# Performance work log

Measured on AMD Instinct MI355X. Metric: run time of the kernel, lower is better.

The kernel has to match this reference:

```python
import jax, jax.numpy as jnp
import numpy as np
import math

B, S, D = 2, 2048, 1024
H = 16
HD = D // H          # 64
ROT = HD             # rotary_pct = 1.0 -> full head dim
BASE = 10000.0


def _rotate_half(x):
    half = x.shape[-1] // 2
    return jnp.concatenate([-x[..., half:], x[..., :half]], axis=-1)


def _cos_sin(seq_len, dtype):
    inv_freq = 1.0 / (BASE ** (jnp.arange(0, ROT, 2, dtype=jnp.float32) / ROT))
    t = jnp.arange(seq_len, dtype=jnp.float32)
    freqs = jnp.einsum('i,j->ij', t, inv_freq)            # [S, ROT/2]
    emb = jnp.concatenate([freqs, freqs], axis=-1)        # [S, ROT]
    return jnp.cos(emb).astype(dtype)[None, None], jnp.sin(emb).astype(dtype)[None, None]


def setup_inputs() -> dict:
    key = jax.random.key(0)
    k1, k2, k3 = jax.random.split(key, 3)
    x = jax.random.normal(k1, (B, S, D), dtype=jnp.float32)
    attn_mask = jnp.ones((B, S), dtype=jnp.int32)
    W_qkv = jax.random.normal(k2, (3 * D, D), dtype=jnp.float32) * 0.02
    W_out = jax.random.normal(k3, (D, D), dtype=jnp.float32) * 0.02
    return {"x": x, "attn_mask": attn_mask, "W_qkv": W_qkv, "W_out": W_out}


def reference(x, attn_mask, W_qkv, W_out):
    bsz, seq_len, _ = x.shape
    dtype = x.dtype
    neg = jnp.finfo(dtype).min

    qkv = jnp.einsum('bsd,ed->bse', x, W_qkv)                     # [B,S,3D]
    qkv = qkv.reshape(bsz, seq_len, 3, H, HD).transpose(2, 0, 3, 1, 4)
    q, k, v = qkv[0], qkv[1], qkv[2]                              # [B,H,S,HD]

    cos, sin = _cos_sin(seq_len, dtype)                           # [1,1,S,ROT]
    q = q * cos + _rotate_half(q) * sin
    k = k * cos + _rotate_half(k) * sin

    scores = jnp.einsum('bhqd,bhkd->bhqk', q, k) / math.sqrt(HD)  # [B,H,S,S]
    causal = jnp.tril(jnp.ones((seq_len, seq_len), dtype=bool))
    scores = jnp.where(causal[None, None], scores, neg)
    # 2D padding mask over key positions
    scores = jnp.where((attn_mask[:, None, None, :] == 0), neg, scores)

    attn = jax.nn.softmax(scores, axis=-1)
    out = jnp.einsum('bhqk,bhkd->bhqd', attn, v)                  # [B,H,S,HD]
    out = out.transpose(0, 2, 1, 3).reshape(bsz, seq_len, D)
    return jnp.einsum('bsd,ed->bse', out, W_out)
```

## Files before the change

kernel.cpp:

```cpp
#include <hip/hip_runtime.h>
#include <hip/hip_bf16.h>
#include <math.h>
#include <stdint.h>

typedef __hip_bfloat16 bf16;
typedef __attribute__((ext_vector_type(8))) short short8;
typedef __attribute__((ext_vector_type(4))) float f32x4;
typedef __attribute__((ext_vector_type(16))) float f32x16;

#define NB 2
#define NS 2048
#define ND 1024
#define NH 16
#define NHD 64
#define N3D 3072

#define SM_SCALE 0.18033688011112042f

__device__ __forceinline__ void gload16(const bf16* g, void* l) {
  __builtin_amdgcn_global_load_lds(
      (const __attribute__((address_space(1))) uint32_t*)g,
      (__attribute__((address_space(3))) uint32_t*)l, 16, 0, 0);
}

__global__ void cast3_kernel(const float4* __restrict__ x, bf16* __restrict__ xb,
                             const float4* __restrict__ wq, bf16* __restrict__ wqb,
                             const float4* __restrict__ wo, bf16* __restrict__ wob) {
  int i = blockIdx.x * blockDim.x + threadIdx.x;
  const float4* src;
  bf16* dst;
  int off;
  if (i < 1048576) {
    src = x; dst = xb; off = i;
  } else if (i < 1835008) {
    src = wq; dst = wqb; off = i - 1048576;
  } else {
    src = wo; dst = wob; off = i - 1835008;
  }
  float4 v = src[off];
  alignas(8) bf16 r[4];
  r[0] = __float2bfloat16(v.x);
  r[1] = __float2bfloat16(v.y);
  r[2] = __float2bfloat16(v.z);
  r[3] = __float2bfloat16(v.w);
  *reinterpret_cast<uint2*>(dst + (size_t)off * 4) = *reinterpret_cast<const uint2*>(r);
}

__global__ void ropetab_kernel(float* __restrict__ cs_tab, float* __restrict__ sn_tab) {
  int idx = blockIdx.x * blockDim.x + threadIdx.x;
  int j = idx & 31;
  int s = idx >> 5;
  float inv = exp2f((float)(2 * j) * (-13.287712379549449f / 64.0f));
  float ang = (float)s * inv;
  float sn, cs;
  sincosf(ang, &sn, &cs);
  cs_tab[idx] = cs;
  sn_tab[idx] = sn;
}

#define GEMM_PIPE_BODY(...)                                                               \
  __shared__ short As[3][128 * 64];                                                       \
  __shared__ short Bs[3][128 * 64];                                                       \
  const int tid = threadIdx.x;                                                            \
  const int lane = tid & 63;                                                              \
  const int w = tid >> 6;                                                                 \
  const int wm = w >> 2, wn = w & 3;                                                      \
  const int l15 = lane & 15, l4 = lane >> 4;                                              \
  const int r0 = tid >> 3, seg = tid & 7;                                                 \
  const int sw = ((seg ^ (r0 & 7)) << 3);                                                 \
  const bf16* Ar0 = Ap + (size_t)(bm0 + r0) * 1024 + sw;                                  \
  const bf16* Ar1 = Ap + (size_t)(bm0 + r0 + 64) * 1024 + sw;                             \
  const bf16* Br0 = Bp + (size_t)(bn0 + r0) * 1024 + sw;                                  \
  const bf16* Br1 = Bp + (size_t)(bn0 + r0 + 64) * 1024 + sw;                             \
  f32x4 acc[4][2] = {};                                                                   \
  gload16(Ar0 + 0, &As[0][w * 512]);                                                      \
  gload16(Ar1 + 0, &As[0][4096 + w * 512]);                                               \
  gload16(Br0 + 0, &Bs[0][w * 512]);                                                      \
  gload16(Br1 + 0, &Bs[0][4096 + w * 512]);                                               \
  gload16(Ar0 + 64, &As[1][w * 512]);                                                     \
  gload16(Ar1 + 64, &As[1][4096 + w * 512]);                                              \
  gload16(Br0 + 64, &Bs[1][w * 512]);                                                     \
  gload16(Br1 + 64, &Bs[1][4096 + w * 512]);                                              \
  asm volatile("s_waitcnt vmcnt(4)" ::: "memory");                                        \
  __builtin_amdgcn_s_barrier();                                                           \
  for (int t = 0; t < 16; ++t) {                                                          \
    const int slot = t % 3;                                                               \
    if (t + 2 < 16) {                                                                     \
      const int ns = (t + 2) % 3;                                                         \
      const int nk = (t + 2) * 64;                                                        \
      gload16(Ar0 + nk, &As[ns][w * 512]);                                                \
      gload16(Ar1 + nk, &As[ns][4096 + w * 512]);                                         \
      gload16(Br0 + nk, &Bs[ns][w * 512]);                                                \
      gload16(Br1 + nk, &Bs[ns][4096 + w * 512]);                                         \
    }                                                                                     \
    _Pragma("unroll") for (int kk = 0; kk < 2; ++kk) {                                    \
      short8 af[4], bfr[2];                                                               \
      _Pragma("unroll") for (int mi = 0; mi < 4; ++mi) {                                  \
        int row = wm * 64 + mi * 16 + l15;                                                \
        af[mi] = *(const short8*)&As[slot][row * 64 + (((kk * 4 + l4) ^ (row & 7)) << 3)];\
      }                                                                                   \
      _Pragma("unroll") for (int ni = 0; ni < 2; ++ni) {                                  \
        int row = (wn >> 1) * 64 + (wn & 1) * 16 + ni * 32 + l15;                         \
        bfr[ni] = *(const short8*)&Bs[slot][row * 64 + (((kk * 4 + l4) ^ (row & 7)) << 3)];\
      }                                                                                   \
      __builtin_amdgcn_s_setprio(1);                                                      \
      _Pragma("unroll") for (int mi = 0; mi < 4; ++mi)                                    \
        _Pragma("unroll") for (int ni = 0; ni < 2; ++ni)                                  \
          acc[mi][ni] =                                                                   \
              __builtin_amdgcn_mfma_f32_16x16x32_bf16(af[mi], bfr[ni], acc[mi][ni], 0, 0, 0);\
      __builtin_amdgcn_s_setprio(0);                                                      \
    }                                                                                     \
    if (t + 2 < 16) {                                                                     \
      asm volatile("s_waitcnt vmcnt(4)" ::: "memory");                                    \
      __builtin_amdgcn_s_barrier();                                                       \
    } else if (t < 15) {                                                                  \
      asm volatile("s_waitcnt vmcnt(0)" ::: "memory");                                    \
      __builtin_amdgcn_s_barrier();                                                       \
    }                                                                                     \
  }                                                                                       \
  __VA_ARGS__

__global__ __launch_bounds__(512) void gemm_qkv(const bf16* __restrict__ Ap,
                                                const bf16* __restrict__ Bp,
                                                const float* __restrict__ cs_tab,
                                                const float* __restrict__ sn_tab,
                                                bf16* __restrict__ Qr, bf16* __restrict__ Kr,
                                                bf16* __restrict__ Vt) {
  const int lin = blockIdx.x;
  const int xcd = lin & 7, idx = lin >> 3;
  const int bxx = (xcd & 1) * 12 + idx % 12;
  const int byy = (xcd >> 1) * 8 + idx / 12;
  const int bn0 = bxx * 128, bm0 = byy * 128;
  GEMM_PIPE_BODY(
    const int colw = bn0 + (wn >> 1) * 64 + (wn & 1) * 16;
    if (bn0 < 2048) {
      bf16* dst = (colw >> 10) ? Kr : Qr;
      const int h = (colw & 1023) >> 6;
      const int j = (wn & 1) * 16 + l15;
      _Pragma("unroll") for (int mi = 0; mi < 4; ++mi) {
        _Pragma("unroll") for (int r = 0; r < 4; ++r) {
          int row = bm0 + wm * 64 + mi * 16 + l4 * 4 + r;
          int b = row >> 11;
          int s = row & (NS - 1);
          float cs = cs_tab[s * 32 + j];
          float sn = sn_tab[s * 32 + j];
          float v0 = acc[mi][0][r];
          float v1 = acc[mi][1][r];
          size_t base = ((size_t)(b * NH + h) * NS + s) * NHD + j;
          dst[base] = __float2bfloat16(v0 * cs - v1 * sn);
          dst[base + 32] = __float2bfloat16(v1 * cs + v0 * sn);
        }
      }
    } else {
      __syncthreads();
      bf16* vtile = reinterpret_cast<bf16*>(&As[0][0]);
      _Pragma("unroll") for (int mi = 0; mi < 4; ++mi) {
        _Pragma("unroll") for (int ni = 0; ni < 2; ++ni) {
          _Pragma("unroll") for (int r = 0; r < 4; ++r) {
            int srow = wm * 64 + mi * 16 + l4 * 4 + r;
            int c = (wn >> 1) * 64 + (wn & 1) * 16 + ni * 32 + l15;
            vtile[c * 136 + srow] = __float2bfloat16(acc[mi][ni][r]);
          }
        }
      }
      __syncthreads();
      const int b_ = bm0 >> 11;
      const int s0 = (bm0 & (NS - 1)) + (tid & 3) * 32;
      const int c = tid >> 2;
      const int head = ((bn0 - 2048) >> 6) + (c >> 6);
      bf16* dstp = Vt + (((size_t)(b_ * NH + head)) * NHD + (c & 63)) * NS + s0;
      _Pragma("unroll") for (int g = 0; g < 4; ++g)
        *reinterpret_cast<short8*>(dstp + g * 8) =
            *reinterpret_cast<const short8*>(&vtile[c * 136 + (tid & 3) * 32 + g * 8]);
    }
  )
}

__global__ __launch_bounds__(512) void gemm_bt(const bf16* __restrict__ Ap,
                                               const bf16* __restrict__ Bp,
                                               float* __restrict__ Cv) {
  const int lin = blockIdx.x;
  const int xcd = lin & 7, idx = lin >> 3;
  const int bxx = (xcd & 1) * 4 + (idx & 3);
  const int byy = (xcd >> 1) * 8 + (idx >> 2);
  const int bn0 = bxx * 128, bm0 = byy * 128;
  GEMM_PIPE_BODY(
    _Pragma("unroll") for (int mi = 0; mi < 4; ++mi) {
      _Pragma("unroll") for (int ni = 0; ni < 2; ++ni) {
        _Pragma("unroll") for (int r = 0; r < 4; ++r) {
          int row = bm0 + wm * 64 + mi * 16 + l4 * 4 + r;
          int col = bn0 + (wn >> 1) * 64 + (wn & 1) * 16 + ni * 32 + l15;
          Cv[(size_t)row * ND + col] = acc[mi][ni][r];
        }
      }
    }
  )
}

__global__ void maskbias_kernel(const int* __restrict__ amask, float* __restrict__ mb, int n) {
  int i = blockIdx.x * blockDim.x + threadIdx.x;
  if (i < n) mb[i] = amask[i] ? 0.f : -1e30f;
}

__global__ __launch_bounds__(256, 2) void attn_kernel(const bf16* __restrict__ Qr,
                                                      const bf16* __restrict__ Kr,
                                                      const bf16* __restrict__ Vt,
                                                      const float* __restrict__ mb,
                                                      bf16* __restrict__ AO) {
  __shared__ short Ks[2][64 * 64];
  __shared__ short Vs[2][64 * 64];
  __shared__ float Mb[2][64];

  const int tid = threadIdx.x;
  const int lane = tid & 63;
  const int w = tid >> 6;
  const int q = lane & 31;
  const int hi = lane >> 5;

  const int lin = blockIdx.x;
  const int xcd = lin & 7;
  const int k = lin >> 3;
  const int bh = xcd * 4 + (k & 3);
  const int kk = k >> 2;
  const int tile = (k < 32) ? (15 - kk) : (kk - 8);
  const int b = bh >> 4, h = bh & 15;
  const int qw = tile * 128 + w * 32;
  const int nc = 2 * tile + 2;

  const bf16* Qb = Qr + (size_t)bh * NS * NHD;
  const bf16* Kb = Kr + (size_t)bh * NS * NHD;
  const bf16* Vb = Vt + (size_t)bh * NHD * NS;

  const int srow = tid >> 2;
  const int sc0 = (tid & 3) * 16;
  const int swz = (srow & 7) << 3;

  short8 Qf[4];
#pragma unroll
  for (int s = 0; s < 4; ++s)
    Qf[s] = *reinterpret_cast<const short8*>(&Qb[(size_t)(qw + q) * NHD + s * 16 + hi * 8]);

  f32x16 o0 = {}, o1 = {};
  float mx = -1e30f, lsum = 0.f;

  short8 kreg[2], vreg[2];
  float4 mreg;
  auto prefetch = [&](int kv0) {
    kreg[0] = *reinterpret_cast<const short8*>(&Kb[(size_t)(kv0 + srow) * NHD + sc0]);
    kreg[1] = *reinterpret_cast<const short8*>(&Kb[(size_t)(kv0 + srow) * NHD + sc0 + 8]);
    vreg[0] = *reinterpret_cast<const short8*>(&Vb[(size_t)srow * NS + kv0 + sc0]);
    vreg[1] = *reinterpret_cast<const short8*>(&Vb[(size_t)srow * NS + kv0 + sc0 + 8]);
    if (tid < 16) mreg = *reinterpret_cast<const float4*>(&mb[b * NS + kv0 + tid * 4]);
  };
  auto stage = [&](int buf) {
    *reinterpret_cast<short8*>(&Ks[buf][srow * 64 + (sc0 ^ swz)]) = kreg[0];
    *reinterpret_cast<short8*>(&Ks[buf][srow * 64 + ((sc0 + 8) ^ swz)]) = kreg[1];
    *reinterpret_cast<short8*>(&Vs[buf][srow * 64 + (sc0 ^ swz)]) = vreg[0];
    *reinterpret_cast<short8*>(&Vs[buf][srow * 64 + ((sc0 + 8) ^ swz)]) = vreg[1];
    if (tid < 16) *reinterpret_cast<float4*>(&Mb[buf][tid * 4]) = mreg;
  };

  prefetch(0);
  stage(0);
  __syncthreads();

  const int rsw = (q & 7) << 3;

  for (int c = 0; c < nc; ++c) {
    const int cur = c & 1;
    const int kv0 = c * 64;
    if (c + 1 < nc) prefetch((c + 1) * 64);

    if (kv0 < qw + 32) {
      f32x16 a0 = {}, a1 = {};
#pragma unroll
      for (int s = 0; s < 4; ++s) {
        short8 kf0 = *reinterpret_cast<const short8*>(
            &Ks[cur][q * 64 + ((s * 16 + hi * 8) ^ rsw)]);
        short8 kf1 = *reinterpret_cast<const short8*>(
            &Ks[cur][(32 + q) * 64 + ((s * 16 + hi * 8) ^ rsw)]);
        a0 = __builtin_amdgcn_mfma_f32_32x32x16_bf16(kf0, Qf[s], a0, 0, 0, 0);
        a1 = __builtin_amdgcn_mfma_f32_32x32x16_bf16(kf1, Qf[s], a1, 0, 0, 0);
      }

      float4 bv[2][4];
#pragma unroll
      for (int t = 0; t < 2; ++t)
#pragma unroll
        for (int g = 0; g < 4; ++g)
          bv[t][g] = *reinterpret_cast<const float4*>(&Mb[cur][t * 32 + g * 8 + hi * 4]);
      const int qg = qw + q;
#pragma unroll
      for (int t = 0; t < 2; ++t) {
        f32x16& a = t ? a1 : a0;
        const bool needc = (kv0 + t * 32 + 31 > qw);
#pragma unroll
        for (int r = 0; r < 16; ++r) {
          float v = fmaf(a[r], SM_SCALE, ((const float*)&bv[t][r >> 2])[r & 3]);
          if (needc) {
            int kvg = kv0 + t * 32 + (r & 3) + 8 * (r >> 2) + 4 * hi;
            if (kvg > qg) v = -1e30f;
          }
          a[r] = v;
        }
      }

      float cm = a0[0];
#pragma unroll
      for (int r = 1; r < 16; ++r) cm = fmaxf(cm, a0[r]);
#pragma unroll
      for (int r = 0; r < 16; ++r) cm = fmaxf(cm, a1[r]);
      float pm = fmaxf(cm, __shfl_xor(cm, 32));

      if (!__all(pm <= mx + 8.f)) {
        float mn = fmaxf(mx, pm);
        float fac = __builtin_amdgcn_exp2f(mx - mn);
        mx = mn;
        lsum *= fac;
#pragma unroll
        for (int r = 0; r < 16; ++r) {
          float fq = __shfl(fac, (r & 3) + 8 * (r >> 2) + 4 * hi);
          o0[r] *= fq;
          o1[r] *= fq;
        }
      }

      float rs = 0.f;
      short8 pa[4];
#pragma unroll
      for (int t = 0; t < 2; ++t) {
        f32x16& a = t ? a1 : a0;
#pragma unroll
        for (int r = 0; r < 16; ++r) {
          float e = __builtin_amdgcn_exp2f(a[r] - mx);
          a[r] = e;
          rs += e;
        }
#pragma unroll
        for (int g = 0; g < 2; ++g) {
          union { unsigned int u; __hip_bfloat162 h2; } X, X2, Y, Y2;
          X.h2 = __float22bfloat162_rn(float2{a[g * 8 + 0], a[g * 8 + 1]});
          X2.h2 = __float22bfloat162_rn(float2{a[g * 8 + 2], a[g * 8 + 3]});
          Y.h2 = __float22bfloat162_rn(float2{a[g * 8 + 4], a[g * 8 + 5]});
          Y2.h2 = __float22bfloat162_rn(float2{a[g * 8 + 6], a[g * 8 + 7]});
          asm volatile("v_permlane32_swap_b32 %0, %1" : "+v"(X.u), "+v"(Y.u));
          asm volatile("v_permlane32_swap_b32 %0, %1" : "+v"(X2.u), "+v"(Y2.u));
          union { unsigned int u[4]; short8 s; } P;
          P.u[0] = X.u;
          P.u[1] = X2.u;
          P.u[2] = Y.u;
          P.u[3] = Y2.u;
          pa[t * 2 + g] = P.s;
        }
      }
      lsum += rs + __shfl_xor(rs, 32);

#pragma unroll
      for (int ks = 0; ks < 4; ++ks) {
        const int vcol = (ks * 16 + hi * 8) ^ rsw;
        short8 vf0 = *reinterpret_cast<const short8*>(&Vs[cur][q * 64 + vcol]);
        short8 vf1 = *reinterpret_cast<const short8*>(&Vs[cur][(32 + q) * 64 + vcol]);
        o0 = __builtin_amdgcn_mfma_f32_32x32x16_bf16(pa[ks], vf0, o0, 0, 0, 0);
        o1 = __builtin_amdgcn_mfma_f32_32x32x16_bf16(pa[ks], vf1, o1, 0, 0, 0);
      }
    }

    if (c + 1 < nc) stage(cur ^ 1);
    __syncthreads();
  }

  float inv = 1.0f / lsum;
#pragma unroll
  for (int r = 0; r < 16; ++r) {
    const int crow = (r & 3) + 8 * (r >> 2) + 4 * hi;
    float iq = __shfl(inv, crow);
    size_t base = (size_t)(b * NS + qw + crow) * ND + h * NHD;
    AO[base + q] = __float2bfloat16(o0[r] * iq);
    AO[base + 32 + q] = __float2bfloat16(o1[r] * iq);
  }
}

extern "C" void kernel_launch(void* const* d_in, const int* in_sizes, int n_in,
                              void* d_out, int out_size, void* d_ws, size_t ws_size,
                              hipStream_t stream) {
  const float* x = (const float*)d_in[0];
  const int* amask = (const int*)d_in[1];
  const float* Wqkv = (const float*)d_in[2];
  const float* Wout = (const float*)d_in[3];
  float* out = (float*)d_out;

  char* p = (char*)d_ws;
  bf16* xb = (bf16*)(p);
  bf16* wqkvb = (bf16*)(p + 8388608);
  bf16* woutb = (bf16*)(p + 14680064);
  float* cs_tab = (float*)(p + 25165824);
  float* sn_tab = (float*)(p + 25427968);
  float* mbias = (float*)(p + 25690112);
  bf16* Qr = (bf16*)(p + 41943040);
  bf16* Kr = (bf16*)(p + 50331648);
  bf16* Vt = (bf16*)(p + 58720256);
  bf16* AO = xb;

  cast3_kernel<<<8192, 256, 0, stream>>>((const float4*)x, xb, (const float4*)Wqkv, wqkvb,
                                         (const float4*)Wout, woutb);
  ropetab_kernel<<<256, 256, 0, stream>>>(cs_tab, sn_tab);

  gemm_qkv<<<768, 512, 0, stream>>>(xb, wqkvb, cs_tab, sn_tab, Qr, Kr, Vt);
  maskbias_kernel<<<16, 256, 0, stream>>>(amask, mbias, NB * NS);
  attn_kernel<<<512, 256, 0, stream>>>(Qr, Kr, Vt, mbias, AO);
  gemm_bt<<<256, 512, 0, stream>>>(AO, woutb, out);
}
```

Measured before the change: 132.3 us.

## Compute Q, K and V tiles per block to reuse the shared A tile

The QKV projection kernel is rewritten so each block loads one 128-row activation tile and the matching 128-column slices of the Q, K and V weights, computing all three outputs together with a 128x384 tile. The launch drops from 768 to 256 blocks, and the activation tile is loaded once instead of three times. The pipeline changes from triple to double buffering with a full vmcnt(0) wait every step. The cost is a 128KB LDS footprint and three times the accumulator registers, which cuts occupancy and gives fewer blocks than the GPU's compute units.

Measured after the change: 120.3 us. 1.1x faster.

```diff
diff --git a/kernel.cpp b/kernel.cpp
--- a/kernel.cpp
+++ b/kernel.cpp
@@ -56,6 +56,134 @@
   sincosf(ang, &sn, &cs);
   cs_tab[idx] = cs;
   sn_tab[idx] = sn;
+}
+
+__global__ __launch_bounds__(512) void gemm_qkv(const bf16* __restrict__ Ap,
+                                                const bf16* __restrict__ Bp,
+                                                const float* __restrict__ cs_tab,
+                                                const float* __restrict__ sn_tab,
+                                                bf16* __restrict__ Qr, bf16* __restrict__ Kr,
+                                                bf16* __restrict__ Vt) {
+  __shared__ short L[2][32768];
+  const int tid = threadIdx.x;
+  const int lane = tid & 63;
+  const int w = tid >> 6;
+  const int wm = w >> 2, wn = w & 3;
+  const int l15 = lane & 15, l4 = lane >> 4;
+  const int lin = blockIdx.x;
+  const int xcd = lin & 7, t2 = lin >> 3;
+  const int byy = (xcd << 2) | (t2 & 3);
+  const int g = t2 >> 2;
+  const int bm0 = byy * 128;
+  const int bn0 = g * 128;
+
+  const int rw = lane >> 3, sg = lane & 7;
+  const int swseg = (sg ^ rw) * 8;
+  const int reg = w >> 1;
+  const int rowb = (w & 1) * 64 + rw;
+  const bf16* srcbase;
+  if (reg == 0)
+    srcbase = Ap + (size_t)(bm0 + rowb) * 1024 + swseg;
+  else
+    srcbase = Bp + (size_t)((reg - 1) * 1024 + bn0 + rowb) * 1024 + swseg;
+  const int ldsb = w * 4096;
+
+  f32x4 acc[3][4][2] = {};
+
+  auto issue = [&](int t) {
+    short* dst = &L[t & 1][ldsb];
+    const bf16* s = srcbase + t * 64;
+#pragma unroll
+    for (int j = 0; j < 8; ++j) gload16(s + (size_t)j * 8 * 1024, dst + j * 512);
+  };
+
+  issue(0);
+  asm volatile("s_waitcnt vmcnt(0)" ::: "memory");
+  __builtin_amdgcn_s_barrier();
+
+  for (int t = 0; t < 16; ++t) {
+    const short* S = L[t & 1];
+    if (t + 1 < 16) issue(t + 1);
+#pragma unroll
+    for (int kk = 0; kk < 2; ++kk) {
+      short8 af[4];
+#pragma unroll
+      for (int mi = 0; mi < 4; ++mi) {
+        int row = wm * 64 + mi * 16 + l15;
+        af[mi] = *(const short8*)&S[row * 64 + (((kk * 4 + l4) ^ (row & 7)) << 3)];
+      }
+#pragma unroll
+      for (int tt = 0; tt < 3; ++tt) {
+        short8 bfr[2];
+#pragma unroll
+        for (int ni = 0; ni < 2; ++ni) {
+          int row = (wn >> 1) * 64 + (wn & 1) * 16 + ni * 32 + l15;
+          bfr[ni] = *(const short8*)&S[(1 + tt) * 8192 + row * 64 +
+                                       (((kk * 4 + l4) ^ (row & 7)) << 3)];
+        }
+        __builtin_amdgcn_s_setprio(1);
+#pragma unroll
+        for (int mi = 0; mi < 4; ++mi)
+#pragma unroll
+          for (int ni = 0; ni < 2; ++ni)
+            acc[tt][mi][ni] = __builtin_amdgcn_mfma_f32_16x16x32_bf16(
+                af[mi], bfr[ni], acc[tt][mi][ni], 0, 0, 0);
+        __builtin_amdgcn_s_setprio(0);
+      }
+    }
+    if (t + 1 < 16) {
+      asm volatile("s_waitcnt vmcnt(0)" ::: "memory");
+      __builtin_amdgcn_s_barrier();
+    }
+  }
+
+  {
+    const int j = (wn & 1) * 16 + l15;
+    const int hq = g * 2 + (wn >> 1);
+#pragma unroll
+    for (int tt = 0; tt < 2; ++tt) {
+      bf16* dst = tt ? Kr : Qr;
+#pragma unroll
+      for (int mi = 0; mi < 4; ++mi)
+#pragma unroll
+        for (int r = 0; r < 4; ++r) {
+          int row = bm0 + wm * 64 + mi * 16 + l4 * 4 + r;
+          int b = row >> 11;
+          int s = row & (NS - 1);
+          float cs = cs_tab[s * 32 + j];
+          float sn = sn_tab[s * 32 + j];
+          float v0 = acc[tt][mi][0][r];
+          float v1 = acc[tt][mi][1][r];
+          size_t base = ((size_t)(b * NH + hq) * NS + s) * NHD + j;
+          dst[base] = __float2bfloat16(v0 * cs - v1 * sn);
+          dst[base + 32] = __float2bfloat16(v1 * cs + v0 * sn);
+        }
+    }
+  }
+  __syncthreads();
+  {
+    bf16* vtile = reinterpret_cast<bf16*>(&L[0][0]);
+#pragma unroll
+    for (int mi = 0; mi < 4; ++mi)
+#pragma unroll
+      for (int ni = 0; ni < 2; ++ni)
+#pragma unroll
+        for (int r = 0; r < 4; ++r) {
+          int srow = wm * 64 + mi * 16 + l4 * 4 + r;
+          int c = (wn >> 1) * 64 + (wn & 1) * 16 + ni * 32 + l15;
+          vtile[c * 136 + srow] = __float2bfloat16(acc[2][mi][ni][r]);
+        }
+    __syncthreads();
+    const int b_ = bm0 >> 11;
+    const int s0 = (bm0 & (NS - 1)) + (tid & 3) * 32;
+    const int c = tid >> 2;
+    const int head = g * 2 + (c >> 6);
+    bf16* dstp = Vt + (((size_t)(b_ * NH + head)) * NHD + (c & 63)) * NS + s0;
+#pragma unroll
+    for (int gg = 0; gg < 4; ++gg)
+      *reinterpret_cast<short8*>(dstp + gg * 8) =
+          *reinterpret_cast<const short8*>(&vtile[c * 136 + (tid & 3) * 32 + gg * 8]);
+  }
 }
 
 #define GEMM_PIPE_BODY(...)                                                               \
@@ -120,62 +248,6 @@
   }                                                                                       \
   __VA_ARGS__
 
-__global__ __launch_bounds__(512) void gemm_qkv(const bf16* __restrict__ Ap,
-                                                const bf16* __restrict__ Bp,
-                                                const float* __restrict__ cs_tab,
-                                                const float* __restrict__ sn_tab,
-                                                bf16* __restrict__ Qr, bf16* __restrict__ Kr,
-                                                bf16* __restrict__ Vt) {
-  const int lin = blockIdx.x;
-  const int xcd = lin & 7, idx = lin >> 3;
-  const int bxx = (xcd & 1) * 12 + idx % 12;
-  const int byy = (xcd >> 1) * 8 + idx / 12;
-  const int bn0 = bxx * 128, bm0 = byy * 128;
-  GEMM_PIPE_BODY(
-    const int colw = bn0 + (wn >> 1) * 64 + (wn & 1) * 16;
-    if (bn0 < 2048) {
-      bf16* dst = (colw >> 10) ? Kr : Qr;
-      const int h = (colw & 1023) >> 6;
-      const int j = (wn & 1) * 16 + l15;
-      _Pragma("unroll") for (int mi = 0; mi < 4; ++mi) {
-        _Pragma("unroll") for (int r = 0; r < 4; ++r) {
-          int row = bm0 + wm * 64 + mi * 16 + l4 * 4 + r;
-          int b = row >> 11;
-          int s = row & (NS - 1);
-          float cs = cs_tab[s * 32 + j];
-          float sn = sn_tab[s * 32 + j];
-          float v0 = acc[mi][0][r];
-          float v1 = acc[mi][1][r];
-          size_t base = ((size_t)(b * NH + h) * NS + s) * NHD + j;
-          dst[base] = __float2bfloat16(v0 * cs - v1 * sn);
-          dst[base + 32] = __float2bfloat16(v1 * cs + v0 * sn);
-        }
-      }
-    } else {
-      __syncthreads();
-      bf16* vtile = reinterpret_cast<bf16*>(&As[0][0]);
-      _Pragma("unroll") for (int mi = 0; mi < 4; ++mi) {
-        _Pragma("unroll") for (int ni = 0; ni < 2; ++ni) {
-          _Pragma("unroll") for (int r = 0; r < 4; ++r) {
-            int srow = wm * 64 + mi * 16 + l4 * 4 + r;
-            int c = (wn >> 1) * 64 + (wn & 1) * 16 + ni * 32 + l15;
-            vtile[c * 136 + srow] = __float2bfloat16(acc[mi][ni][r]);
-          }
-        }
-      }
-      __syncthreads();
-      const int b_ = bm0 >> 11;
-      const int s0 = (bm0 & (NS - 1)) + (tid & 3) * 32;
-      const int c = tid >> 2;
-      const int head = ((bn0 - 2048) >> 6) + (c >> 6);
-      bf16* dstp = Vt + (((size_t)(b_ * NH + head)) * NHD + (c & 63)) * NS + s0;
-      _Pragma("unroll") for (int g = 0; g < 4; ++g)
-        *reinterpret_cast<short8*>(dstp + g * 8) =
-            *reinterpret_cast<const short8*>(&vtile[c * 136 + (tid & 3) * 32 + g * 8]);
-    }
-  )
-}
-
 __global__ __launch_bounds__(512) void gemm_bt(const bf16* __restrict__ Ap,
                                                const bf16* __restrict__ Bp,
                                                float* __restrict__ Cv) {
@@ -405,7 +477,7 @@
                                          (const float4*)Wout, woutb);
   ropetab_kernel<<<256, 256, 0, stream>>>(cs_tab, sn_tab);
 
-  gemm_qkv<<<768, 512, 0, stream>>>(xb, wqkvb, cs_tab, sn_tab, Qr, Kr, Vt);
+  gemm_qkv<<<256, 512, 0, stream>>>(xb, wqkvb, cs_tab, sn_tab, Qr, Kr, Vt);
   maskbias_kernel<<<16, 256, 0, stream>>>(amask, mbias, NB * NS);
   attn_kernel<<<512, 256, 0, stream>>>(Qr, Kr, Vt, mbias, AO);
   gemm_bt<<<256, 512, 0, stream>>>(AO, woutb, out);
```
